# Performance work log

Hardware: AMD Instinct MI355X
Metric: run time of the kernel (lower is better)

Reference implementation:

```python
import jax, jax.numpy as jnp
import numpy as np

MODEL = 1024
HEADS = 16
HEAD_DIM = MODEL // HEADS
INNER = 4096
EPS = 1e-5


def _layer_norm(x, gamma, beta):
    mu = jnp.mean(x, axis=-1, keepdims=True)
    var = jnp.mean((x - mu) ** 2, axis=-1, keepdims=True)
    return (x - mu) * jax.lax.rsqrt(var + EPS) * gamma + beta


def setup_inputs() -> dict:
    key = jax.random.key(0)
    ks = jax.random.split(key, 12)
    B, S = 4, 2048
    s_in = 1.0 / np.sqrt(MODEL)
    s_ff = 1.0 / np.sqrt(INNER)
    return {
        "x": jax.random.normal(ks[0], (B, S, MODEL), jnp.float32),
        "mask": jnp.ones((B, 1, 1, S), jnp.int32),
        "Wq": jax.random.normal(ks[1], (MODEL, MODEL), jnp.float32) * s_in,
        "bq": jnp.zeros((MODEL,), jnp.float32),
        "Wk": jax.random.normal(ks[2], (MODEL, MODEL), jnp.float32) * s_in,
        "bk": jnp.zeros((MODEL,), jnp.float32),
        "Wv": jax.random.normal(ks[3], (MODEL, MODEL), jnp.float32) * s_in,
        "bv": jnp.zeros((MODEL,), jnp.float32),
        "Wo": jax.random.normal(ks[4], (MODEL, MODEL), jnp.float32) * s_in,
        "bo": jnp.zeros((MODEL,), jnp.float32),
        "g1": jnp.ones((MODEL,), jnp.float32),
        "beta1": jnp.zeros((MODEL,), jnp.float32),
        "W1": jax.random.normal(ks[5], (MODEL, INNER), jnp.float32) * s_in,
        "b1": jnp.zeros((INNER,), jnp.float32),
        "W2": jax.random.normal(ks[6], (INNER, MODEL), jnp.float32) * s_ff,
        "b2": jnp.zeros((MODEL,), jnp.float32),
        "g2": jnp.ones((MODEL,), jnp.float32),
        "beta2": jnp.zeros((MODEL,), jnp.float32),
    }


def reference(x, mask, Wq, bq, Wk, bk, Wv, bv, Wo, bo, g1, beta1, W1, b1, W2, b2, g2, beta2):
    B, S, _ = x.shape
    temp = jnp.sqrt(jnp.float32(HEAD_DIM))
    # projections -> [B, H, S, Dh]
    q = (x @ Wq + bq).reshape(B, S, HEADS, HEAD_DIM).transpose(0, 2, 1, 3)
    k = (x @ Wk + bk).reshape(B, S, HEADS, HEAD_DIM).transpose(0, 2, 1, 3)
    v = (x @ Wv + bv).reshape(B, S, HEADS, HEAD_DIM).transpose(0, 2, 1, 3)
    # scores [B, H, S, S]
    scores = jnp.einsum("bhqd,bhkd->bhqk", q / temp, k)
    scores = jnp.where(mask == 0, jnp.float32(-1e10), scores)
    attn = jax.nn.softmax(scores, axis=-1)
    ctx = jnp.einsum("bhqk,bhkd->bhqd", attn, v)
    ctx = ctx.transpose(0, 2, 1, 3).reshape(B, S, MODEL)
    attn_out = ctx @ Wo + bo
    x = _layer_norm(x + attn_out, g1, beta1)
    ff = jax.nn.relu(x @ W1 + b1) @ W2 + b2
    x = _layer_norm(x + ff, g2, beta2)
    return x
```

## Files before the change

### kernel.cpp

```cpp
#include <hip/hip_runtime.h>
#include <stdint.h>

#define MODEL 1024
#define INNER 4096
#define NHEADS 16
#define HDIM 64
#define BATCH 4
#define SEQ 2048
#define MROWS (BATCH*SEQ)

#define QSCALE 0.18033688011112042f

typedef __bf16 bf16x8 __attribute__((ext_vector_type(8)));
typedef float f32x4 __attribute__((ext_vector_type(4)));
typedef float f32x16 __attribute__((ext_vector_type(16)));
typedef unsigned short ushort4v __attribute__((ext_vector_type(4)));
typedef unsigned uint4v __attribute__((ext_vector_type(4)));

extern "C" __device__ float __ocml_native_exp2_f32(float);

__device__ __forceinline__ unsigned short f2bf(float f) {
  unsigned u = __builtin_bit_cast(unsigned, f);
  u += 0x7FFFu + ((u >> 16) & 1u);
  return (unsigned short)(u >> 16);
}
__device__ __forceinline__ float bf2f(unsigned short u) {
  return __builtin_bit_cast(float, (unsigned)u << 16);
}
__device__ __forceinline__ unsigned packbf_trunc(float lo, float hi) {
  return __builtin_amdgcn_perm(__builtin_bit_cast(unsigned, hi),
                               __builtin_bit_cast(unsigned, lo), 0x07060302u);
}

#define AS1 __attribute__((address_space(1)))
#define AS3 __attribute__((address_space(3)))
__device__ __forceinline__ void gload_lds16(const void* g, void* l) {
  __builtin_amdgcn_global_load_lds((const AS1 void*)g, (AS3 void*)l, 16, 0, 0);
}

__global__ __launch_bounds__(256) void k_cvt(const float* __restrict__ in,
                                             unsigned short* __restrict__ out, int n4) {
  int i = blockIdx.x * 256 + threadIdx.x;
  if (i < n4) {
    float4 v = ((const float4*)in)[i];
    ushort4v o = { f2bf(v.x), f2bf(v.y), f2bf(v.z), f2bf(v.w) };
    ((ushort4v*)out)[i] = o;
  }
}

__global__ __launch_bounds__(256) void k_bcat(const float* __restrict__ bq,
                                              const float* __restrict__ bk,
                                              const float* __restrict__ bv,
                                              float* __restrict__ o) {
  int i = blockIdx.x * 256 + threadIdx.x;
  o[i] = (i < 1024) ? bq[i] : (i < 2048) ? bk[i - 1024] : bv[i - 2048];
}

__global__ __launch_bounds__(256) void k_transpose(const float* __restrict__ W,
                                                   unsigned short* __restrict__ Wt,
                                                   int K, int N) {
  __shared__ float tile[32][33];
  const int n0 = blockIdx.x * 32, k0 = blockIdx.y * 32;
  const int c = threadIdx.x & 31, r4 = threadIdx.x >> 5;
#pragma unroll
  for (int i = 0; i < 4; i++) {
    int r = r4 + i * 8;
    tile[r][c] = W[(size_t)(k0 + r) * N + n0 + c];
  }
  __syncthreads();
#pragma unroll
  for (int i = 0; i < 4; i++) {
    int r = r4 + i * 8;
    Wt[(size_t)(n0 + r) * K + k0 + c] = f2bf(tile[c][r]);
  }
}

template <int MODE, bool SPLIT>
__global__ __launch_bounds__(512, 2) void k_gemm(const unsigned short* __restrict__ A,
                                                 const unsigned short* __restrict__ Bt,
                                                 const float* __restrict__ bias,
                                                 void* __restrict__ out0,
                                                 void* __restrict__ out1,
                                                 void* __restrict__ out2,
                                                 int M, int N, int Kfull) {
  __shared__ unsigned short As[3 * 256 * 32];
  __shared__ unsigned short Bs[3 * 256 * 32];
  const int t = threadIdx.x;
  const int lane = t & 63;
  const int w = t >> 6;
  const int li = lane & 15, lg = lane >> 4;
  const int wm8 = w >> 2, wn4 = w & 3;

  const unsigned nwg = gridDim.x * gridDim.y;
  const unsigned lin = blockIdx.y * gridDim.x + blockIdx.x;
  const unsigned q8 = nwg >> 3, r8 = nwg & 7, xcd = lin & 7, pos = lin >> 3;
  const unsigned swz = (xcd < r8 ? xcd * (q8 + 1) : r8 * (q8 + 1) + (xcd - r8) * q8) + pos;
  int bx = swz % gridDim.x, by = swz / gridDim.x;

  int kp = 0, Ksub = Kfull;
  if (SPLIT) {
    const int hx = gridDim.x >> 1;
    kp = bx >= hx;
    bx -= kp * hx;
    Ksub = Kfull >> 1;
  }
  const int bm = by * 256, bn = bx * 256;
  const size_t koff = (size_t)kp * Ksub;
  const int NT = Ksub / 32;

  const int sr0 = w * 16 + (lane >> 2);
  const int sr1 = sr0 + 128;
  const int sl = lane & 3;
  const unsigned short* pA0 = A + (size_t)(bm + sr0) * Kfull + koff + ((sl ^ ((sr0 >> 1) & 3)) << 3);
  const unsigned short* pA1 = A + (size_t)(bm + sr1) * Kfull + koff + ((sl ^ ((sr1 >> 1) & 3)) << 3);
  const unsigned short* pB0 = Bt + (size_t)(bn + sr0) * Kfull + koff + ((sl ^ ((sr0 >> 1) & 3)) << 3);
  const unsigned short* pB1 = Bt + (size_t)(bn + sr1) * Kfull + koff + ((sl ^ ((sr1 >> 1) & 3)) << 3);

  f32x4 acc[8][4] = {};

  auto stageA = [&](int buf, int tt) {
    gload_lds16(pA0 + tt * 32, &As[buf * 8192 + w * 512]);
    gload_lds16(pA1 + tt * 32, &As[buf * 8192 + 4096 + w * 512]);
  };
  auto stageB = [&](int buf, int tt) {
    gload_lds16(pB0 + tt * 32, &Bs[buf * 8192 + w * 512]);
    gload_lds16(pB1 + tt * 32, &Bs[buf * 8192 + 4096 + w * 512]);
  };

  stageA(0, 0); stageB(0, 0);
  stageA(1, 1); stageB(1, 1);
  asm volatile("s_waitcnt vmcnt(4)" ::: "memory");
  __builtin_amdgcn_s_barrier();

  int buf = 0;
  for (int tt = 0; tt < NT; ++tt) {
    const int nb = (buf + 2 >= 3) ? buf - 1 : buf + 2;
    const unsigned short* Ab = &As[buf * 8192];
    const unsigned short* Bb = &Bs[buf * 8192];
    bf16x8 av[4], bv_[4];
#pragma unroll
    for (int m = 0; m < 4; m++) {
      const int r = wm8 * 128 + m * 16 + li;
      av[m] = *(const bf16x8*)&Ab[r * 32 + ((lg ^ ((r >> 1) & 3)) << 3)];
    }
#pragma unroll
    for (int n = 0; n < 4; n++) {
      const int r = wn4 * 64 + n * 16 + li;
      bv_[n] = *(const bf16x8*)&Bb[r * 32 + ((lg ^ ((r >> 1) & 3)) << 3)];
    }
    if (tt + 2 < NT) stageA(nb, tt + 2);
    __builtin_amdgcn_s_barrier();
    __builtin_amdgcn_s_setprio(1);
#pragma unroll
    for (int m = 0; m < 4; m++)
#pragma unroll
      for (int n = 0; n < 4; n++)
        acc[m][n] = __builtin_amdgcn_mfma_f32_16x16x32_bf16(av[m], bv_[n], acc[m][n], 0, 0, 0);
    __builtin_amdgcn_s_setprio(0);
    bf16x8 av2[4];
#pragma unroll
    for (int m = 0; m < 4; m++) {
      const int r = wm8 * 128 + 64 + m * 16 + li;
      av2[m] = *(const bf16x8*)&Ab[r * 32 + ((lg ^ ((r >> 1) & 3)) << 3)];
    }
    if (tt + 2 < NT) stageB(nb, tt + 2);
    __builtin_amdgcn_s_barrier();
    __builtin_amdgcn_s_setprio(1);
#pragma unroll
    for (int m = 0; m < 4; m++)
#pragma unroll
      for (int n = 0; n < 4; n++)
        acc[m + 4][n] = __builtin_amdgcn_mfma_f32_16x16x32_bf16(av2[m], bv_[n], acc[m + 4][n], 0, 0, 0);
    __builtin_amdgcn_s_setprio(0);
    if (tt + 2 < NT) asm volatile("s_waitcnt vmcnt(4)" ::: "memory");
    else             asm volatile("s_waitcnt vmcnt(0)" ::: "memory");
    __builtin_amdgcn_s_barrier();
    buf = (buf == 2) ? 0 : buf + 1;
  }

#pragma unroll
  for (int m = 0; m < 8; m++) {
    const int row0 = bm + wm8 * 128 + m * 16 + lg * 4;
#pragma unroll
    for (int n = 0; n < 4; n++) {
      const int gcol = bn + wn4 * 64 + n * 16 + li;
      if (MODE == 0) {
        unsigned short* dst = (unsigned short*)(kp ? out1 : out0);
        const float bvc = (kp == 0) ? bias[gcol] : 0.f;
#pragma unroll
        for (int j = 0; j < 4; j++)
          dst[(size_t)(row0 + j) * N + gcol] = f2bf(acc[m][n][j] + bvc);
      } else if (MODE == 2) {
        const float bvc = bias[gcol];
#pragma unroll
        for (int j = 0; j < 4; j++)
          ((unsigned short*)out0)[(size_t)(row0 + j) * N + gcol] = f2bf(fmaxf(acc[m][n][j] + bvc, 0.f));
      } else {
        const float bvc = bias[gcol];
        const int region = gcol >> 10, lcol = gcol & 1023;
        if (region < 2) {
          unsigned short* dst = (unsigned short*)(region ? out1 : out0);
          const float sc = region ? 1.f : QSCALE;
#pragma unroll
          for (int j = 0; j < 4; j++)
            dst[(size_t)(row0 + j) * MODEL + lcol] = f2bf((acc[m][n][j] + bvc) * sc);
        } else {
          ushort4v o = {f2bf(acc[m][n][0] + bvc), f2bf(acc[m][n][1] + bvc),
                        f2bf(acc[m][n][2] + bvc), f2bf(acc[m][n][3] + bvc)};
          *(ushort4v*)&((unsigned short*)out2)[(size_t)lcol * MROWS + row0] = o;
        }
      }
    }
  }
}

__global__ __launch_bounds__(256, 4) void k_attn(const unsigned short* __restrict__ q,
                                                 const unsigned short* __restrict__ kptr,
                                                 const unsigned short* __restrict__ vt,
                                                 const int* __restrict__ mask,
                                                 unsigned short* __restrict__ ctx) {
  __shared__ unsigned short Ks[2][64 * 64];
  __shared__ unsigned short Vs[2][64 * 64];
  __shared__ unsigned maskw[SEQ / 32];
  const int t = threadIdx.x, lane = t & 63, w = t >> 6;
  const int l31 = lane & 31, hi = lane >> 5;
  const int bh = blockIdx.y, b = bh >> 4, h = bh & 15;
  const int q0 = blockIdx.x * 128;
  const size_t basebs = (size_t)b * SEQ;
  const int srow = lane >> 3;
  const int scsw = ((lane & 7) ^ srow) * 8;

  {
    const int base = b * SEQ + t * 8;
    int4 m0 = *(const int4*)&mask[base];
    int4 m1 = *(const int4*)&mask[base + 4];
    unsigned byte = (unsigned)(m0.x != 0) | ((unsigned)(m0.y != 0) << 1) |
                    ((unsigned)(m0.z != 0) << 2) | ((unsigned)(m0.w != 0) << 3) |
                    ((unsigned)(m1.x != 0) << 4) | ((unsigned)(m1.y != 0) << 5) |
                    ((unsigned)(m1.z != 0) << 6) | ((unsigned)(m1.w != 0) << 7);
    ((unsigned char*)maskw)[t] = (unsigned char)byte;
  }
  __syncthreads();

  auto stageKV = [&](int buf, int kt) {
#pragma unroll
    for (int i = 0; i < 2; i++) {
      const int row = i * 32 + w * 8 + srow;
      gload_lds16(kptr + (basebs + kt + row) * MODEL + h * 64 + scsw,
                  &Ks[buf][i * 2048 + w * 512]);
    }
#pragma unroll
    for (int i = 0; i < 2; i++) {
      const int row = i * 32 + w * 8 + srow;
      gload_lds16(vt + (size_t)(h * 64 + row) * MROWS + basebs + kt + scsw,
                  &Vs[buf][i * 2048 + w * 512]);
    }
  };

  stageKV(0, 0);

  bf16x8 qf[4];
#pragma unroll
  for (int s = 0; s < 4; s++)
    qf[s] = *(const bf16x8*)&q[(basebs + q0 + w * 32 + l31) * MODEL + h * 64 + s * 16 + hi * 8];

  f32x16 acc_o[2] = {};
  float lrow = 0.f;

  int cur = 0;
  for (int kt = 0; kt < SEQ; kt += 64) {
    if (kt + 64 < SEQ) {
      stageKV(cur ^ 1, kt + 64);
      asm volatile("s_waitcnt vmcnt(4)" ::: "memory");
    } else {
      asm volatile("s_waitcnt vmcnt(0)" ::: "memory");
    }
    __builtin_amdgcn_s_barrier();

    f32x16 sacc[2] = {};
    __builtin_amdgcn_s_setprio(1);
#pragma unroll
    for (int kb = 0; kb < 2; kb++) {
#pragma unroll
      for (int s = 0; s < 4; s++) {
        bf16x8 kf = *(const bf16x8*)&Ks[cur][(kb * 32 + l31) * 64 + (((s * 2 + hi) ^ (l31 & 7)) << 3)];
        sacc[kb] = __builtin_amdgcn_mfma_f32_32x32x16_bf16(kf, qf[s], sacc[kb], 0, 0, 0);
      }
    }
    __builtin_amdgcn_s_setprio(0);

    const unsigned W0 = maskw[(kt >> 5)], W1 = maskw[(kt >> 5) + 1];
    if ((W0 & W1) != 0xFFFFFFFFu) {
#pragma unroll
      for (int kb = 0; kb < 2; kb++) {
        const unsigned Wb = kb ? W1 : W0;
#pragma unroll
        for (int rq = 0; rq < 4; rq++)
#pragma unroll
          for (int e = 0; e < 4; e++) {
            const int r = rq * 4 + e;
            sacc[kb][r] = ((Wb >> (e + 8 * rq + 4 * hi)) & 1u) ? sacc[kb][r] : -1e30f;
          }
      }
    }

    unsigned pk[2][8];
    float tsum = 0.f;
#pragma unroll
    for (int kb = 0; kb < 2; kb++)
#pragma unroll
      for (int i = 0; i < 8; i++) {
        float p0 = __ocml_native_exp2_f32(sacc[kb][2 * i]);
        float p1 = __ocml_native_exp2_f32(sacc[kb][2 * i + 1]);
        tsum += p0 + p1;
        pk[kb][i] = packbf_trunc(p0, p1);
      }
    {
      float ta = tsum, tb = tsum;
      asm("v_permlane32_swap_b32 %0, %1" : "+v"(ta), "+v"(tb));
      lrow += ta + tb;
    }

    __builtin_amdgcn_s_setprio(1);
#pragma unroll
    for (int kb = 0; kb < 2; kb++) {
#pragma unroll
      for (int s = 0; s < 2; s++) {
        unsigned a0 = pk[kb][4 * s + 0], a2 = pk[kb][4 * s + 2];
        asm("v_permlane32_swap_b32 %0, %1" : "+v"(a0), "+v"(a2));
        unsigned a1 = pk[kb][4 * s + 1], a3 = pk[kb][4 * s + 3];
        asm("v_permlane32_swap_b32 %0, %1" : "+v"(a1), "+v"(a3));
        uint4v pu = {a0, a1, a2, a3};
        bf16x8 paf = __builtin_bit_cast(bf16x8, pu);
#pragma unroll
        for (int db = 0; db < 2; db++) {
          bf16x8 vf = *(const bf16x8*)&Vs[cur][(db * 32 + l31) * 64 + (((kb * 4 + s * 2 + hi) ^ (l31 & 7)) << 3)];
          acc_o[db] = __builtin_amdgcn_mfma_f32_32x32x16_bf16(vf, paf, acc_o[db], 0, 0, 0);
        }
      }
    }
    __builtin_amdgcn_s_setprio(0);
    __builtin_amdgcn_sched_barrier(0);
    __builtin_amdgcn_s_barrier();
    cur ^= 1;
  }

  const float rl = 1.f / lrow;
  const size_t rowoff = (basebs + q0 + w * 32 + l31) * (size_t)MODEL + h * 64;
#pragma unroll
  for (int db = 0; db < 2; db++)
#pragma unroll
    for (int rq = 0; rq < 4; rq++) {
      const int r = rq * 4;
      ushort4v o = {f2bf(acc_o[db][r] * rl), f2bf(acc_o[db][r + 1] * rl),
                    f2bf(acc_o[db][r + 2] * rl), f2bf(acc_o[db][r + 3] * rl)};
      *(ushort4v*)&ctx[rowoff + db * 32 + rq * 8 + 4 * hi] = o;
    }
}

template <bool AF32>
__global__ __launch_bounds__(256) void k_ln(const void* __restrict__ a,
                                            const unsigned short* __restrict__ b0,
                                            const unsigned short* __restrict__ b1,
                                            const float* __restrict__ gamma,
                                            const float* __restrict__ beta,
                                            float* __restrict__ outf,
                                            unsigned short* __restrict__ outb) {
  const int row = blockIdx.x;
  const int t = threadIdx.x;
  const size_t off = (size_t)row * MODEL + t * 4;
  float4 xa;
  if (AF32) {
    xa = *(const float4*)((const float*)a + off);
  } else {
    ushort4v av = *(const ushort4v*)((const unsigned short*)a + off);
    xa = {bf2f(av.x), bf2f(av.y), bf2f(av.z), bf2f(av.w)};
  }
  ushort4v u0 = *(const ushort4v*)&b0[off];
  ushort4v u1 = *(const ushort4v*)&b1[off];
  float z0 = xa.x + bf2f(u0.x) + bf2f(u1.x);
  float z1 = xa.y + bf2f(u0.y) + bf2f(u1.y);
  float z2 = xa.z + bf2f(u0.z) + bf2f(u1.z);
  float z3 = xa.w + bf2f(u0.w) + bf2f(u1.w);
  float s = z0 + z1 + z2 + z3;
  float ss = z0 * z0 + z1 * z1 + z2 * z2 + z3 * z3;
#pragma unroll
  for (int o = 1; o < 64; o <<= 1) { s += __shfl_xor(s, o); ss += __shfl_xor(ss, o); }
  __shared__ float red[8];
  const int lane = t & 63, w = t >> 6;
  if (lane == 0) { red[w] = s; red[4 + w] = ss; }
  __syncthreads();
  s = red[0] + red[1] + red[2] + red[3];
  ss = red[4] + red[5] + red[6] + red[7];
  float mu = s * (1.f / MODEL);
  float var = ss * (1.f / MODEL) - mu * mu;
  float inv = rsqrtf(var + 1e-5f);
  float4 g = *(const float4*)&gamma[t * 4];
  float4 be = *(const float4*)&beta[t * 4];
  float o0 = (z0 - mu) * inv * g.x + be.x;
  float o1 = (z1 - mu) * inv * g.y + be.y;
  float o2 = (z2 - mu) * inv * g.z + be.z;
  float o3 = (z3 - mu) * inv * g.w + be.w;
  if (AF32) {
    ushort4v ob = {f2bf(o0), f2bf(o1), f2bf(o2), f2bf(o3)};
    *(ushort4v*)&outb[off] = ob;
  } else {
    float4 ov = {o0, o1, o2, o3};
    *(float4*)&outf[off] = ov;
  }
}

extern "C" void kernel_launch(void* const* d_in, const int* in_sizes, int n_in,
                              void* d_out, int out_size, void* d_ws, size_t ws_size,
                              hipStream_t stream) {
  (void)in_sizes; (void)n_in; (void)out_size; (void)ws_size;
  const float* x   = (const float*)d_in[0];
  const int*   mask= (const int*)d_in[1];
  const float* Wq  = (const float*)d_in[2];
  const float* bq  = (const float*)d_in[3];
  const float* Wk  = (const float*)d_in[4];
  const float* bk  = (const float*)d_in[5];
  const float* Wv  = (const float*)d_in[6];
  const float* bv  = (const float*)d_in[7];
  const float* Wo  = (const float*)d_in[8];
  const float* bo  = (const float*)d_in[9];
  const float* g1  = (const float*)d_in[10];
  const float* be1 = (const float*)d_in[11];
  const float* W1  = (const float*)d_in[12];
  const float* b1  = (const float*)d_in[13];
  const float* W2  = (const float*)d_in[14];
  const float* b2  = (const float*)d_in[15];
  const float* g2  = (const float*)d_in[16];
  const float* be2 = (const float*)d_in[17];
  float* out = (float*)d_out;

  char* p = (char*)d_ws;
  auto alloc = [&](size_t bytes) { char* r = p; p += (bytes + 255) & ~(size_t)255; return r; };
  unsigned short* xb    = (unsigned short*)alloc((size_t)MROWS * MODEL * 2);
  unsigned short* y1b   = (unsigned short*)alloc((size_t)MROWS * MODEL * 2);
  unsigned short* WqkvT = (unsigned short*)alloc((size_t)3 * MODEL * MODEL * 2);
  unsigned short* WoT   = (unsigned short*)alloc((size_t)MODEL * MODEL * 2);
  unsigned short* W1T   = (unsigned short*)alloc((size_t)MODEL * INNER * 2);
  unsigned short* W2T   = (unsigned short*)alloc((size_t)INNER * MODEL * 2);
  float* bqkv           = (float*)alloc(3072 * 4);
  unsigned short* qb    = (unsigned short*)alloc((size_t)MROWS * MODEL * 2);
  unsigned short* kb    = (unsigned short*)alloc((size_t)MROWS * MODEL * 2);
  unsigned short* vtb   = (unsigned short*)alloc((size_t)MODEL * MROWS * 2);
  unsigned short* ctxb  = (unsigned short*)alloc((size_t)MROWS * MODEL * 2);
  unsigned short* ao0   = (unsigned short*)alloc((size_t)MROWS * MODEL * 2);
  unsigned short* ao1   = (unsigned short*)alloc((size_t)MROWS * MODEL * 2);
  unsigned short* h1  = qb;
  unsigned short* ff0 = ao0;
  unsigned short* ff1 = ao1;

  k_cvt<<<(MROWS * MODEL / 4) / 256, 256, 0, stream>>>(x, xb, MROWS * MODEL / 4);
  k_bcat<<<12, 256, 0, stream>>>(bq, bk, bv, bqkv);
  k_transpose<<<dim3(MODEL / 32, MODEL / 32), 256, 0, stream>>>(Wq, WqkvT, MODEL, MODEL);
  k_transpose<<<dim3(MODEL / 32, MODEL / 32), 256, 0, stream>>>(Wk, WqkvT + (size_t)MODEL * MODEL, MODEL, MODEL);
  k_transpose<<<dim3(MODEL / 32, MODEL / 32), 256, 0, stream>>>(Wv, WqkvT + (size_t)2 * MODEL * MODEL, MODEL, MODEL);
  k_transpose<<<dim3(MODEL / 32, MODEL / 32), 256, 0, stream>>>(Wo, WoT, MODEL, MODEL);
  k_transpose<<<dim3(INNER / 32, MODEL / 32), 256, 0, stream>>>(W1, W1T, MODEL, INNER);
  k_transpose<<<dim3(MODEL / 32, INNER / 32), 256, 0, stream>>>(W2, W2T, INNER, MODEL);

  k_gemm<3, false><<<dim3(12, MROWS / 256), 512, 0, stream>>>(xb, WqkvT, bqkv, qb, kb, vtb, MROWS, 3072, MODEL);

  k_attn<<<dim3(SEQ / 128, BATCH * NHEADS), 256, 0, stream>>>(qb, kb, vtb, mask, ctxb);

  k_gemm<0, true><<<dim3(8, MROWS / 256), 512, 0, stream>>>(ctxb, WoT, bo, ao0, ao1, nullptr, MROWS, MODEL, MODEL);

  k_ln<true><<<MROWS, 256, 0, stream>>>(x, ao0, ao1, g1, be1, nullptr, y1b);

  k_gemm<2, false><<<dim3(INNER / 256, MROWS / 256), 512, 0, stream>>>(y1b, W1T, b1, h1, nullptr, nullptr, MROWS, INNER, MODEL);

  k_gemm<0, true><<<dim3(8, MROWS / 256), 512, 0, stream>>>(h1, W2T, b2, ff0, ff1, nullptr, MROWS, MODEL, INNER);

  k_ln<false><<<MROWS, 256, 0, stream>>>(y1b, ff0, ff1, g2, be2, out, nullptr);
}
```

Baseline: 401.4 us.

## Restructure GEMM mainloop to double-buffered K=64 tiles with quarter-split staging

The bf16 GEMM mainloop changes from a triple-buffered K=32 pipeline to a double-buffered K=64 tile with an 8-way XOR swizzle. Each tile's loads are split into four parts (A/B halves) that are interleaved between four MFMA quadrant groups. The intent is to issue more MFMAs per barrier and per LDS load, and to spread global-to-LDS copies across the compute phases. The more intricate vmcnt and barrier schedule risks races or stalls if the wait counts are off. Register pressure also rises from the larger fragment sets.

After: 378.1 us. 5.8% less time.

```diff
diff --git a/kernel.cpp b/kernel.cpp
--- a/kernel.cpp
+++ b/kernel.cpp
@@ -83,8 +83,8 @@
                                                  void* __restrict__ out1,
                                                  void* __restrict__ out2,
                                                  int M, int N, int Kfull) {
-  __shared__ unsigned short As[3 * 256 * 32];
-  __shared__ unsigned short Bs[3 * 256 * 32];
+  __shared__ unsigned short As[2 * 256 * 64];
+  __shared__ unsigned short Bs[2 * 256 * 64];
   const int t = threadIdx.x;
   const int lane = t & 63;
   const int w = t >> 6;
@@ -106,76 +106,100 @@
   }
   const int bm = by * 256, bn = bx * 256;
   const size_t koff = (size_t)kp * Ksub;
-  const int NT = Ksub / 32;
-
-  const int sr0 = w * 16 + (lane >> 2);
-  const int sr1 = sr0 + 128;
-  const int sl = lane & 3;
-  const unsigned short* pA0 = A + (size_t)(bm + sr0) * Kfull + koff + ((sl ^ ((sr0 >> 1) & 3)) << 3);
-  const unsigned short* pA1 = A + (size_t)(bm + sr1) * Kfull + koff + ((sl ^ ((sr1 >> 1) & 3)) << 3);
-  const unsigned short* pB0 = Bt + (size_t)(bn + sr0) * Kfull + koff + ((sl ^ ((sr0 >> 1) & 3)) << 3);
-  const unsigned short* pB1 = Bt + (size_t)(bn + sr1) * Kfull + koff + ((sl ^ ((sr1 >> 1) & 3)) << 3);
+  const int NI = Ksub / 128;
+
+  const int srow = lane >> 3, ssl = lane & 7;
+  const int scol = (ssl ^ srow) << 3;
+  const unsigned short* pA = A + (size_t)(bm + w * 8 + srow) * Kfull + koff + scol;
+  const unsigned short* pB = Bt + (size_t)(bn + w * 8 + srow) * Kfull + koff + scol;
+
+  auto stage = [&](int kt, int part) {
+    const int buf = kt & 1;
+    const bool isA = part >= 2;
+    const int half = part & 1;
+    const unsigned short* src = (isA ? pA : pB) + (size_t)(half * 128) * Kfull + kt * 64;
+    unsigned short* dst = (isA ? (unsigned short*)As : (unsigned short*)Bs)
+                          + buf * 16384 + half * 8192 + w * 512;
+    gload_lds16(src, dst);
+    gload_lds16(src + (size_t)64 * Kfull, dst + 4096);
+  };
 
   f32x4 acc[8][4] = {};
 
-  auto stageA = [&](int buf, int tt) {
-    gload_lds16(pA0 + tt * 32, &As[buf * 8192 + w * 512]);
-    gload_lds16(pA1 + tt * 32, &As[buf * 8192 + 4096 + w * 512]);
+  auto rdA = [&](bf16x8 a[4][2], int buf, int mq) {
+#pragma unroll
+    for (int m = 0; m < 4; m++) {
+      const int r = wm8 * 128 + mq * 64 + m * 16 + li;
+#pragma unroll
+      for (int kk = 0; kk < 2; kk++)
+        a[m][kk] = *(const bf16x8*)&As[buf * 16384 + r * 64 + (((kk * 4 + lg) ^ (r & 7)) << 3)];
+    }
   };
-  auto stageB = [&](int buf, int tt) {
-    gload_lds16(pB0 + tt * 32, &Bs[buf * 8192 + w * 512]);
-    gload_lds16(pB1 + tt * 32, &Bs[buf * 8192 + 4096 + w * 512]);
+  auto rdB = [&](bf16x8 bb[2][2], int buf, int nq) {
+#pragma unroll
+    for (int n = 0; n < 2; n++) {
+      const int r = wn4 * 64 + nq * 32 + n * 16 + li;
+#pragma unroll
+      for (int kk = 0; kk < 2; kk++)
+        bb[n][kk] = *(const bf16x8*)&Bs[buf * 16384 + r * 64 + (((kk * 4 + lg) ^ (r & 7)) << 3)];
+    }
   };
-
-  stageA(0, 0); stageB(0, 0);
-  stageA(1, 1); stageB(1, 1);
-  asm volatile("s_waitcnt vmcnt(4)" ::: "memory");
+  auto mf = [&](bf16x8 a[4][2], bf16x8 bb[2][2], int mq, int nq) {
+    __builtin_amdgcn_s_setprio(1);
+#pragma unroll
+    for (int kk = 0; kk < 2; kk++)
+#pragma unroll
+      for (int m = 0; m < 4; m++)
+#pragma unroll
+        for (int n = 0; n < 2; n++)
+          acc[mq * 4 + m][nq * 2 + n] = __builtin_amdgcn_mfma_f32_16x16x32_bf16(
+              a[m][kk], bb[n][kk], acc[mq * 4 + m][nq * 2 + n], 0, 0, 0);
+    __builtin_amdgcn_s_setprio(0);
+  };
+
+  stage(0, 0); stage(0, 1); stage(0, 2); stage(0, 3);
+  stage(1, 0); stage(1, 1); stage(1, 2);
+  asm volatile("s_waitcnt vmcnt(6)" ::: "memory");
   __builtin_amdgcn_s_barrier();
 
-  int buf = 0;
-  for (int tt = 0; tt < NT; ++tt) {
-    const int nb = (buf + 2 >= 3) ? buf - 1 : buf + 2;
-    const unsigned short* Ab = &As[buf * 8192];
-    const unsigned short* Bb = &Bs[buf * 8192];
-    bf16x8 av[4], bv_[4];
-#pragma unroll
-    for (int m = 0; m < 4; m++) {
-      const int r = wm8 * 128 + m * 16 + li;
-      av[m] = *(const bf16x8*)&Ab[r * 32 + ((lg ^ ((r >> 1) & 3)) << 3)];
-    }
-#pragma unroll
-    for (int n = 0; n < 4; n++) {
-      const int r = wn4 * 64 + n * 16 + li;
-      bv_[n] = *(const bf16x8*)&Bb[r * 32 + ((lg ^ ((r >> 1) & 3)) << 3)];
-    }
-    if (tt + 2 < NT) stageA(nb, tt + 2);
-    __builtin_amdgcn_s_barrier();
-    __builtin_amdgcn_s_setprio(1);
-#pragma unroll
-    for (int m = 0; m < 4; m++)
-#pragma unroll
-      for (int n = 0; n < 4; n++)
-        acc[m][n] = __builtin_amdgcn_mfma_f32_16x16x32_bf16(av[m], bv_[n], acc[m][n], 0, 0, 0);
-    __builtin_amdgcn_s_setprio(0);
-    bf16x8 av2[4];
-#pragma unroll
-    for (int m = 0; m < 4; m++) {
-      const int r = wm8 * 128 + 64 + m * 16 + li;
-      av2[m] = *(const bf16x8*)&Ab[r * 32 + ((lg ^ ((r >> 1) & 3)) << 3)];
-    }
-    if (tt + 2 < NT) stageB(nb, tt + 2);
-    __builtin_amdgcn_s_barrier();
-    __builtin_amdgcn_s_setprio(1);
-#pragma unroll
-    for (int m = 0; m < 4; m++)
-#pragma unroll
-      for (int n = 0; n < 4; n++)
-        acc[m + 4][n] = __builtin_amdgcn_mfma_f32_16x16x32_bf16(av2[m], bv_[n], acc[m + 4][n], 0, 0, 0);
-    __builtin_amdgcn_s_setprio(0);
-    if (tt + 2 < NT) asm volatile("s_waitcnt vmcnt(4)" ::: "memory");
-    else             asm volatile("s_waitcnt vmcnt(0)" ::: "memory");
-    __builtin_amdgcn_s_barrier();
-    buf = (buf == 2) ? 0 : buf + 1;
+  for (int i = 0; i < NI; ++i) {
+    const int k1 = 2 * i + 1, k2 = 2 * i + 2, k3 = 2 * i + 3;
+    const bool more = (i < NI - 1);
+    bf16x8 a[4][2], a2[4][2], b0[2][2], b1[2][2];
+    rdA(a, 0, 0); rdB(b0, 0, 0); rdB(b1, 0, 1);
+    stage(k1, 3);
+    __builtin_amdgcn_s_barrier();
+    mf(a, b0, 0, 0);
+    rdA(a2, 0, 1);
+    if (more) stage(k2, 0);
+    __builtin_amdgcn_s_barrier();
+    mf(a, b1, 0, 1);
+    if (more) stage(k2, 1);
+    __builtin_amdgcn_s_barrier();
+    mf(a2, b0, 1, 0);
+    if (more) {
+      stage(k2, 2);
+      asm volatile("s_waitcnt vmcnt(6)" ::: "memory");
+    } else {
+      asm volatile("s_waitcnt vmcnt(0)" ::: "memory");
+    }
+    __builtin_amdgcn_s_barrier();
+    mf(a2, b1, 1, 1);
+    rdA(a, 1, 0); rdB(b0, 1, 0); rdB(b1, 1, 1);
+    if (more) stage(k2, 3);
+    __builtin_amdgcn_s_barrier();
+    mf(a, b0, 0, 0);
+    rdA(a2, 1, 1);
+    if (more) stage(k3, 0);
+    __builtin_amdgcn_s_barrier();
+    mf(a, b1, 0, 1);
+    if (more) stage(k3, 1);
+    __builtin_amdgcn_s_barrier();
+    mf(a2, b0, 1, 0);
+    if (more) stage(k3, 2);
+    asm volatile("s_waitcnt vmcnt(6)" ::: "memory");
+    __builtin_amdgcn_s_barrier();
+    mf(a2, b1, 1, 1);
   }
 
 #pragma unroll
```
